# Kernel optimization log

Measured on AMD Instinct MI355X. Metric: run time of the kernel, lower is better.

Reference implementation:

```python
import jax, jax.numpy as jnp
import numpy as np

# ---- dims (match init_kwargs / input_specs) ----
B, T_H, NR = 32, 128, 1      # batch, rollout horizon t, n_ref (= n_x = n_y)
L, D, H = 6, 128, 4          # n_layer, n_embd, n_head
T = T_H + 1                  # GPT sequence buffer length (U has t+1 entries)
DH = D // H
STD = 0.02


def setup_inputs() -> dict:
    key = jax.random.key(0)
    ks = jax.random.split(key, 16)
    p = {}
    p["data"] = jax.random.uniform(ks[0], (B, 2), jnp.float32)          # plant params p0, p1
    p["r"] = jax.random.normal(ks[1], (B, T_H, NR), jnp.float32)        # reference signal
    # GPT params
    p["wte_w"] = jax.random.normal(ks[2], (2 * NR, D), jnp.float32) * STD
    p["wte_b"] = jnp.zeros((D,), jnp.float32)
    p["wpe"] = jax.random.normal(ks[3], (T, D), jnp.float32) * STD
    p["ln1_w"] = jnp.ones((L, D), jnp.float32)
    p["ln1_b"] = jnp.zeros((L, D), jnp.float32)
    p["ln2_w"] = jnp.ones((L, D), jnp.float32)
    p["ln2_b"] = jnp.zeros((L, D), jnp.float32)
    p["qkv_w"] = jax.random.normal(ks[4], (L, D, 3 * D), jnp.float32) * STD
    p["qkv_b"] = jnp.zeros((L, 3 * D), jnp.float32)
    p["attn_proj_w"] = jax.random.normal(ks[5], (L, D, D), jnp.float32) * STD
    p["attn_proj_b"] = jnp.zeros((L, D), jnp.float32)
    p["fc_w"] = jax.random.normal(ks[6], (L, D, 4 * D), jnp.float32) * STD
    p["fc_b"] = jnp.zeros((L, 4 * D), jnp.float32)
    p["fc2_w"] = jax.random.normal(ks[7], (L, 4 * D, D), jnp.float32) * STD
    p["fc2_b"] = jnp.zeros((L, D), jnp.float32)
    p["lnf_w"] = jnp.ones((D,), jnp.float32)
    p["lnf_b"] = jnp.zeros((D,), jnp.float32)
    p["head_w"] = jax.random.normal(ks[8], (D, NR), jnp.float32) * STD
    p["head_b"] = jnp.zeros((NR,), jnp.float32)
    return p


def _ln(x, w, b):
    m = jnp.mean(x, axis=-1, keepdims=True)
    v = jnp.var(x, axis=-1, keepdims=True)
    return (x - m) * jax.lax.rsqrt(v + 1e-5) * w + b


def reference(data, r, wte_w, wte_b, wpe, ln1_w, ln1_b, ln2_w, ln2_b,
              qkv_w, qkv_b, attn_proj_w, attn_proj_b, fc_w, fc_b,
              fc2_w, fc2_b, lnf_w, lnf_b, head_w, head_b):
    causal = jnp.tril(jnp.ones((T, T), bool))
    scale = 1.0 / np.sqrt(DH)

    def gpt(E, U):
        # E, U: [B, T, NR] zero-padded buffers; causal attention makes pos i
        # depend only on filled positions 0..i (identical to prefix forward).
        x = jnp.concatenate([E, U], axis=-1) @ wte_w + wte_b + wpe[None]  # [B,T,D]
        for l in range(L):
            h = _ln(x, ln1_w[l], ln1_b[l])
            qkv = h @ qkv_w[l] + qkv_b[l]
            q, k, v = jnp.split(qkv, 3, axis=-1)
            q = q.reshape(B, T, H, DH)
            k = k.reshape(B, T, H, DH)
            v = v.reshape(B, T, H, DH)
            att = jnp.einsum('bqhd,bkhd->bhqk', q, k) * scale
            att = jnp.where(causal[None, None], att, -1e9)
            att = jax.nn.softmax(att, axis=-1)
            o = jnp.einsum('bhqk,bkhd->bqhd', att, v).reshape(B, T, D)
            x = x + o @ attn_proj_w[l] + attn_proj_b[l]
            h2 = _ln(x, ln2_w[l], ln2_b[l])
            x = x + jax.nn.gelu(h2 @ fc_w[l] + fc_b[l]) @ fc2_w[l] + fc2_b[l]
        x = _ln(x, lnf_w, lnf_b)
        return x @ head_w + head_b  # [B, T, NR]

    p0 = data[:, 0:1]  # [B,1]
    p1 = data[:, 1:2]

    def step(carry, i):
        E, U, Y, s = carry          # s == y_i == x_i (nx == ny)
        e_i = jnp.take(r, i, axis=1) - s       # [B, NR]
        Y = Y.at[:, i].set(s)
        E = E.at[:, i].set(e_i)
        pred = gpt(E, U)
        u_next = jnp.take(pred, i, axis=1)     # last valid position == i
        U = U.at[:, i + 1].set(u_next)
        # ODE plant: Euler step with Ts = 1
        z = p0 * s                               # intermediate_vars
        x_dot = -z + p1 * jnp.tanh(u_next)       # dynamics
        s_next = s + 1.0 * x_dot
        return (E, U, Y, s_next), None

    E0 = jnp.zeros((B, T, NR), jnp.float32)
    U0 = jnp.zeros((B, T, NR), jnp.float32)    # U[:, 0] = 0
    Y0 = jnp.zeros((B, T_H, NR), jnp.float32)
    s0 = jnp.zeros((B, NR), jnp.float32)
    (E, U, Y, s), _ = jax.lax.scan(step, (E0, U0, Y0, s0), jnp.arange(T_H))
    return Y
```

## Files before the change

### kernel.cpp

```cpp
#include <hip/hip_runtime.h>
#include <math.h>

#define NB   32
#define TH   128
#define NL   6
#define DD   128
#define NH   4
#define DHD  32
#define TCAP 128
#define D3   384
#define D4   512

typedef _Float16 f16;
typedef _Float16 f16x4 __attribute__((ext_vector_type(4)));
typedef _Float16 f16x8 __attribute__((ext_vector_type(8)));

__global__ void prep_kernel(const float* __restrict__ qkv, const float* __restrict__ proj,
                            const float* __restrict__ fc,  const float* __restrict__ fc2,
                            f16* __restrict__ out) {
    int i = blockIdx.x * blockDim.x + threadIdx.x;
    const int n0 = NL * DD * D3, n1 = NL * DD * DD, n2 = NL * DD * D4, n3 = NL * D4 * DD;
    const int total = n0 + n1 + n2 + n3;
    if (i >= total) return;
    float v;
    if (i < n0)                 v = qkv[i];
    else if (i < n0 + n1)       v = proj[i - n0];
    else if (i < n0 + n1 + n2)  v = fc[i - n0 - n1];
    else                        v = fc2[i - n0 - n1 - n2];
    out[i] = (f16)v;
}

template<int CTRL>
__device__ __forceinline__ float dpp_add_f(float v) {
    int t = __builtin_amdgcn_update_dpp(0, __float_as_int(v), CTRL, 0xF, 0xF, true);
    return v + __int_as_float(t);
}
template<int CTRL>
__device__ __forceinline__ float dpp_max_f(float v) {
    int iv = __float_as_int(v);
    int t = __builtin_amdgcn_update_dpp(iv, iv, CTRL, 0xF, 0xF, false);
    return fmaxf(v, __int_as_float(t));
}
__device__ __forceinline__ float wave_sum_bcast(float v) {
    v = dpp_add_f<0x111>(v); v = dpp_add_f<0x112>(v);
    v = dpp_add_f<0x114>(v); v = dpp_add_f<0x118>(v);
    v = dpp_add_f<0x142>(v); v = dpp_add_f<0x143>(v);
    return __int_as_float(__builtin_amdgcn_readlane(__float_as_int(v), 63));
}
__device__ __forceinline__ float wave_max_bcast(float v) {
    v = dpp_max_f<0x111>(v); v = dpp_max_f<0x112>(v);
    v = dpp_max_f<0x114>(v); v = dpp_max_f<0x118>(v);
    v = dpp_max_f<0x142>(v); v = dpp_max_f<0x143>(v);
    return __int_as_float(__builtin_amdgcn_readlane(__float_as_int(v), 63));
}
__device__ __forceinline__ float red8_16_32(float v) {
    v = dpp_add_f<0x108>(v);
    v += __shfl_xor(v, 16);
    v += __shfl_xor(v, 32);
    return v;
}
__device__ __forceinline__ float red4_32(float v) {
    v = dpp_add_f<0x104>(v);
    v = dpp_add_f<0x108>(v);
    v += __shfl_xor(v, 16);
    v += __shfl_xor(v, 32);
    return v;
}

__device__ __forceinline__ float gelu_tanh(float v) {
    float t = v * v * v;
    return 0.5f * v * (1.f + tanhf(0.7978845608028654f * (v + 0.044715f * t)));
}

__device__ __forceinline__ void bar_lds() {
    asm volatile("s_waitcnt lgkmcnt(0)" ::: "memory");
    __builtin_amdgcn_s_barrier();
    asm volatile("" ::: "memory");
}
__device__ __forceinline__ void bar_step() {
    asm volatile("s_waitcnt vmcnt(0) lgkmcnt(0)" ::: "memory");
    __builtin_amdgcn_s_barrier();
    asm volatile("" ::: "memory");
}

__global__ __launch_bounds__(512, 1) void gpt_loop(
    const float* __restrict__ data,  const float* __restrict__ r,
    const float* __restrict__ wte_w, const float* __restrict__ wte_b,
    const float* __restrict__ wpe,
    const float* __restrict__ ln1_w, const float* __restrict__ ln1_b,
    const float* __restrict__ ln2_w, const float* __restrict__ ln2_b,
    const float* __restrict__ qkv_b, const float* __restrict__ proj_b,
    const float* __restrict__ fc_b,  const float* __restrict__ fc2_b,
    const float* __restrict__ lnf_w, const float* __restrict__ lnf_b,
    const float* __restrict__ head_w,const float* __restrict__ head_b,
    const f16* __restrict__ Wq, const f16* __restrict__ Wp,
    const f16* __restrict__ Wf, const f16* __restrict__ Wf2,
    f16* __restrict__ Kc, f16* __restrict__ Vc,
    float* __restrict__ Y)
{
    const int b    = blockIdx.x;
    const int tid  = threadIdx.x;
    const int lane = tid & 63;
    const int wid  = tid >> 6;

    __shared__ __align__(16) float xb[2][DD];
    __shared__ __align__(16) float qv[DD], o[DD], hmid[D4];
    __shared__ __align__(16) float sc[NH][TCAP];
    __shared__ __align__(16) f16 kvK[DD], kvV[DD];
    __shared__ __align__(16) float c_ln1w[NL][DD], c_ln1b[NL][DD], c_ln2w[NL][DD], c_ln2b[NL][DD];
    __shared__ __align__(16) float c_qkvb[NL][D3], c_projb[NL][DD], c_fcb[NL][D4], c_fc2b[NL][DD];
    __shared__ __align__(16) float c_lnfw[DD], c_lnfb[DD], c_headw[DD], c_wte0[DD], c_wte1[DD], c_wteb[DD];

    const float p0 = data[b * 2 + 0];
    const float p1 = data[b * 2 + 1];
    const float hb = head_b[0];

    f16* Kb = Kc + (size_t)b * NL * TCAP * DD;
    f16* Vb = Vc + (size_t)b * NL * TCAP * DD;

    for (int idx = tid; idx < NL * DD; idx += 512) {
        int l = idx / DD, d = idx % DD;
        c_ln1w[l][d] = ln1_w[idx]; c_ln1b[l][d] = ln1_b[idx];
        c_ln2w[l][d] = ln2_w[idx]; c_ln2b[l][d] = ln2_b[idx];
        c_projb[l][d] = proj_b[idx]; c_fc2b[l][d] = fc2_b[idx];
    }
    for (int idx = tid; idx < NL * D3; idx += 512) c_qkvb[idx / D3][idx % D3] = qkv_b[idx];
    for (int idx = tid; idx < NL * D4; idx += 512) c_fcb[idx / D4][idx % D4] = fc_b[idx];
    if (tid < DD) {
        c_lnfw[tid] = lnf_w[tid]; c_lnfb[tid] = lnf_b[tid]; c_headw[tid] = head_w[tid];
        c_wte0[tid] = wte_w[tid]; c_wte1[tid] = wte_w[DD + tid]; c_wteb[tid] = wte_b[tid];
    }
    {
        float4 z4 = make_float4(0.f, 0.f, 0.f, 0.f);
        float4* K4 = (float4*)Kb; float4* V4 = (float4*)Vb;
        const int n4 = NL * TCAP * DD * 2 / 16;
        for (int idx = tid; idx < n4; idx += 512) { K4[idx] = z4; V4[idx] = z4; }
    }
    __syncthreads();

    float s_reg = 0.f;
    if (wid == 0) {
        float e0 = r[b * TH + 0];
        xb[0][lane]      = e0 * c_wte0[lane]      + c_wteb[lane]      + wpe[lane];
        xb[0][lane + 64] = e0 * c_wte0[lane + 64] + c_wteb[lane + 64] + wpe[64 + lane];
    }

    const int cgq = lane & 7, ksq = lane >> 3;
    const int cbq = wid * 64 + cgq * 8, k0q = ksq * 16;
    const int hh  = wid - 4;
    const int vcg = lane & 3, vjs = lane >> 2;
    const int pcg = lane & 31, pks = lane >> 5;
    const int fcg = lane & 15, fks = lane >> 4;

    f16x8 wq[16];
    if (wid < 6) {
        const f16* W = Wq + cbq;
        #pragma unroll
        for (int k = 0; k < 16; k++) wq[k] = *(const f16x8*)(W + (size_t)(k0q + k) * D3);
    }
    __syncthreads();

    for (int i = 0; i < TH; i++) {
        const int inext = (i + 1 < TH) ? (i + 1) : (TH - 1);
        float r_next = r[b * TH + inext];
        float wpe_a  = wpe[(i + 1) * DD + lane];
        float wpe_b  = wpe[(i + 1) * DD + 64 + lane];

        for (int l = 0; l < NL; l++) {
            const int pl = l & 1;
            float* xcur = xb[pl];
            float* xnxt = xb[1 - pl];
            f16* Krow = Kb + ((size_t)l * TCAP + i) * DD;
            f16* Vrow = Vb + ((size_t)l * TCAP + i) * DD;
            const f16* Kl = Kb + (size_t)l * TCAP * DD;
            const f16* Vl = Vb + (size_t)l * TCAP * DD;

            if (wid >= 6) {
                xnxt[(wid - 6) * 64 + lane] = 0.f;
            } else {
                float v0 = xcur[lane], v1 = xcur[lane + 64];
                float sm = wave_sum_bcast(v0 + v1);
                float sq = wave_sum_bcast(v0 * v0 + v1 * v1);
                float m  = sm * (1.f / DD);
                float rs = rsqrtf(sq * (1.f / DD) - m * m + 1e-5f);
                float hk[16];
                #pragma unroll
                for (int t = 0; t < 4; t++) {
                    float4 xx = *(const float4*)&xcur[k0q + 4 * t];
                    float4 ww = *(const float4*)&c_ln1w[l][k0q + 4 * t];
                    float4 bb = *(const float4*)&c_ln1b[l][k0q + 4 * t];
                    hk[4 * t + 0] = (xx.x - m) * rs * ww.x + bb.x;
                    hk[4 * t + 1] = (xx.y - m) * rs * ww.y + bb.y;
                    hk[4 * t + 2] = (xx.z - m) * rs * ww.z + bb.z;
                    hk[4 * t + 3] = (xx.w - m) * rs * ww.w + bb.w;
                }
                float acc[8] = {0.f,0.f,0.f,0.f,0.f,0.f,0.f,0.f};
                #pragma unroll
                for (int k = 0; k < 16; k++) {
                    f16x8 w = wq[k];
                    float hkk = hk[k];
                    #pragma unroll
                    for (int j = 0; j < 8; j++) acc[j] += hkk * (float)w[j];
                }
                #pragma unroll
                for (int j = 0; j < 8; j++) acc[j] = red8_16_32(acc[j]);
                if (ksq == 0) {
                    if (cbq < DD) {
                        #pragma unroll
                        for (int j = 0; j < 8; j++) qv[cbq + j] = acc[j] + c_qkvb[l][cbq + j];
                    } else if (cbq < 2 * DD) {
                        f16x8 kv;
                        #pragma unroll
                        for (int j = 0; j < 8; j++) kv[j] = (f16)(acc[j] + c_qkvb[l][cbq + j]);
                        *(f16x8*)(Krow + (cbq - DD)) = kv;
                        *(f16x8*)(&kvK[cbq - DD])   = kv;
                    } else {
                        f16x8 vv;
                        #pragma unroll
                        for (int j = 0; j < 8; j++) vv[j] = (f16)(acc[j] + c_qkvb[l][cbq + j]);
                        *(f16x8*)(Vrow + (cbq - 2 * DD)) = vv;
                        *(f16x8*)(&kvV[cbq - 2 * DD])   = vv;
                    }
                }
            }
            f16x4 wpt[16];
            if (wid >= 4) {
                const f16* W = Wp + (size_t)l * DD * DD + (size_t)(hh * DHD + pks * 16) * DD + pcg * 4;
                #pragma unroll
                for (int k = 0; k < 16; k++) wpt[k] = *(const f16x4*)(W + (size_t)k * DD);
            }
            bar_lds();

            f16x8 wfh1[8], wfh2[8];
            if (wid < 4) {
                const f16* W2 = Wf + (size_t)l * DD * D4 + cbq;
                #pragma unroll
                for (int k = 0; k < 8; k++) wfh1[k] = *(const f16x8*)(W2 + (size_t)(k0q + k) * D4);
                #pragma unroll
                for (int k = 0; k < 8; k++) wfh2[k] = *(const f16x8*)(W2 + (size_t)(k0q + 8 + k) * D4);
            } else {
                const int im1 = (i > 0) ? (i - 1) : 0;
                const int j0 = (lane < i) ? lane : im1;
                const int j1 = (lane + 64 < i) ? (lane + 64) : im1;
                const f16* K0p = Kl + (size_t)j0 * DD + hh * DHD;
                const f16* K1p = Kl + (size_t)j1 * DD + hh * DHD;
                f16x8 kr0[4], kr1[4];
                #pragma unroll
                for (int g = 0; g < 4; g++) {
                    kr0[g] = *(const f16x8*)(K0p + g * 8);
                    kr1[g] = *(const f16x8*)(K1p + g * 8);
                }
                if (lane == i) {
                    #pragma unroll
                    for (int g = 0; g < 4; g++) kr0[g] = *(const f16x8*)(&kvK[hh * DHD + g * 8]);
                }
                if (lane + 64 == i) {
                    #pragma unroll
                    for (int g = 0; g < 4; g++) kr1[g] = *(const f16x8*)(&kvK[hh * DHD + g * 8]);
                }
                float d0 = 0.f, d1 = 0.f;
                #pragma unroll
                for (int g = 0; g < 4; g++) {
                    f16x8 ka = kr0[g], kb2 = kr1[g];
                    float4 qa = *(const float4*)&qv[hh * DHD + g * 8];
                    float4 qb = *(const float4*)&qv[hh * DHD + g * 8 + 4];
                    d0 += qa.x*(float)ka[0] + qa.y*(float)ka[1] + qa.z*(float)ka[2] + qa.w*(float)ka[3]
                        + qb.x*(float)ka[4] + qb.y*(float)ka[5] + qb.z*(float)ka[6] + qb.w*(float)ka[7];
                    d1 += qa.x*(float)kb2[0] + qa.y*(float)kb2[1] + qa.z*(float)kb2[2] + qa.w*(float)kb2[3]
                        + qb.x*(float)kb2[4] + qb.y*(float)kb2[5] + qb.z*(float)kb2[6] + qb.w*(float)kb2[7];
                }
                f16x8 vreg[8];
                const f16* Vp = Vl + hh * DHD + vcg * 8;
                #pragma unroll
                for (int t = 0; t < 8; t++) {
                    int row = vjs * 8 + t; row = (row < i) ? row : im1;
                    vreg[t] = *(const f16x8*)(Vp + (size_t)row * DD);
                }
                #pragma unroll
                for (int t = 0; t < 8; t++) {
                    if (vjs * 8 + t == i) vreg[t] = *(const f16x8*)(&kvV[hh * DHD + vcg * 8]);
                }
                const float sscale = 0.17677669529663687f;
                const bool ok0 = (lane <= i), ok1 = (lane + 64 <= i);
                float s0 = ok0 ? d0 * sscale : -1e30f;
                float s1 = ok1 ? d1 * sscale : -1e30f;
                float mx = wave_max_bcast(fmaxf(s0, s1));
                float e0 = ok0 ? expf(s0 - mx) : 0.f;
                float e1 = ok1 ? expf(s1 - mx) : 0.f;
                float inv = 1.f / wave_sum_bcast(e0 + e1);
                sc[hh][lane]      = e0 * inv;
                sc[hh][lane + 64] = e1 * inv;
                __builtin_amdgcn_wave_barrier();
                const int ja = vjs * 8;
                float4 pa = *(const float4*)&sc[hh][ja];
                float4 pb = *(const float4*)&sc[hh][ja + 4];
                float pv[8] = {pa.x, pa.y, pa.z, pa.w, pb.x, pb.y, pb.z, pb.w};
                float a[8] = {0.f,0.f,0.f,0.f,0.f,0.f,0.f,0.f};
                #pragma unroll
                for (int t = 0; t < 8; t++) {
                    f16x8 vv = vreg[t];
                    float p = pv[t];
                    #pragma unroll
                    for (int u = 0; u < 8; u++) a[u] += p * (float)vv[u];
                }
                #pragma unroll
                for (int u = 0; u < 8; u++) a[u] = red4_32(a[u]);
                if (vjs == 0) {
                    #pragma unroll
                    for (int u = 0; u < 8; u++) o[hh * DHD + vcg * 8 + u] = a[u];
                }
                __builtin_amdgcn_wave_barrier();
                float ov[16];
                #pragma unroll
                for (int t = 0; t < 4; t++) {
                    float4 q4 = *(const float4*)&o[hh * DHD + pks * 16 + 4 * t];
                    ov[4 * t + 0] = q4.x; ov[4 * t + 1] = q4.y;
                    ov[4 * t + 2] = q4.z; ov[4 * t + 3] = q4.w;
                }
                float ap[4] = {0.f,0.f,0.f,0.f};
                #pragma unroll
                for (int k = 0; k < 16; k++) {
                    f16x4 w = wpt[k];
                    float okk = ov[k];
                    #pragma unroll
                    for (int j = 0; j < 4; j++) ap[j] += okk * (float)w[j];
                }
                #pragma unroll
                for (int j = 0; j < 4; j++) ap[j] += __shfl_xor(ap[j], 32);
                if (pks == 0) {
                    #pragma unroll
                    for (int j = 0; j < 4; j++)
                        atomicAdd(&xcur[pcg * 4 + j],
                                  ap[j] + (hh == 0 ? c_projb[l][pcg * 4 + j] : 0.f));
                }
                const f16* W2 = Wf + (size_t)l * DD * D4 + cbq;
                #pragma unroll
                for (int k = 0; k < 8; k++) wfh1[k] = *(const f16x8*)(W2 + (size_t)(k0q + k) * D4);
                #pragma unroll
                for (int k = 0; k < 8; k++) wfh2[k] = *(const f16x8*)(W2 + (size_t)(k0q + 8 + k) * D4);
            }
            bar_lds();

            {
                float v0 = xcur[lane], v1 = xcur[lane + 64];
                float sm = wave_sum_bcast(v0 + v1);
                float sq = wave_sum_bcast(v0 * v0 + v1 * v1);
                float m  = sm * (1.f / DD);
                float rs = rsqrtf(sq * (1.f / DD) - m * m + 1e-5f);
                float hk[16];
                #pragma unroll
                for (int t = 0; t < 4; t++) {
                    float4 xx = *(const float4*)&xcur[k0q + 4 * t];
                    float4 ww = *(const float4*)&c_ln2w[l][k0q + 4 * t];
                    float4 bb = *(const float4*)&c_ln2b[l][k0q + 4 * t];
                    hk[4 * t + 0] = (xx.x - m) * rs * ww.x + bb.x;
                    hk[4 * t + 1] = (xx.y - m) * rs * ww.y + bb.y;
                    hk[4 * t + 2] = (xx.z - m) * rs * ww.z + bb.z;
                    hk[4 * t + 3] = (xx.w - m) * rs * ww.w + bb.w;
                }
                float acc[8] = {0.f,0.f,0.f,0.f,0.f,0.f,0.f,0.f};
                #pragma unroll
                for (int k = 0; k < 8; k++) {
                    f16x8 w = wfh1[k];
                    float hkk = hk[k];
                    #pragma unroll
                    for (int j = 0; j < 8; j++) acc[j] += hkk * (float)w[j];
                }
                #pragma unroll
                for (int k = 0; k < 8; k++) {
                    f16x8 w = wfh2[k];
                    float hkk = hk[8 + k];
                    #pragma unroll
                    for (int j = 0; j < 8; j++) acc[j] += hkk * (float)w[j];
                }
                f16x8 wf2t[16];
                {
                    const f16* W3 = Wf2 + (size_t)l * D4 * DD + (size_t)(wid * 64 + fks * 16) * DD + fcg * 8;
                    #pragma unroll
                    for (int k = 0; k < 16; k++) wf2t[k] = *(const f16x8*)(W3 + (size_t)k * DD);
                }
                #pragma unroll
                for (int j = 0; j < 8; j++) acc[j] = red8_16_32(acc[j]);
                if (ksq == 0) {
                    #pragma unroll
                    for (int j = 0; j < 8; j++) hmid[cbq + j] = gelu_tanh(acc[j] + c_fcb[l][cbq + j]);
                }
                __builtin_amdgcn_wave_barrier();
                float hv[16];
                #pragma unroll
                for (int t = 0; t < 4; t++) {
                    float4 m4 = *(const float4*)&hmid[wid * 64 + fks * 16 + 4 * t];
                    hv[4 * t + 0] = m4.x; hv[4 * t + 1] = m4.y;
                    hv[4 * t + 2] = m4.z; hv[4 * t + 3] = m4.w;
                }
                float a2[8] = {0.f,0.f,0.f,0.f,0.f,0.f,0.f,0.f};
                #pragma unroll
                for (int k = 0; k < 16; k++) {
                    f16x8 w = wf2t[k];
                    float hkk = hv[k];
                    #pragma unroll
                    for (int j = 0; j < 8; j++) a2[j] += hkk * (float)w[j];
                }
                {
                    const int ln = (l + 1 == NL) ? 0 : (l + 1);
                    if (wid < 6) {
                        const f16* W = Wq + (size_t)ln * DD * D3 + cbq;
                        #pragma unroll
                        for (int k = 0; k < 16; k++) wq[k] = *(const f16x8*)(W + (size_t)(k0q + k) * D3);
                    }
                }
                #pragma unroll
                for (int j = 0; j < 8; j++) {
                    a2[j] += __shfl_xor(a2[j], 16);
                    a2[j] += __shfl_xor(a2[j], 32);
                }
                if (fks == 0) {
                    #pragma unroll
                    for (int j = 0; j < 8; j++)
                        atomicAdd(&xnxt[fcg * 8 + j],
                                  a2[j] + (wid == 0 ? xcur[fcg * 8 + j] + c_fc2b[l][fcg * 8 + j] : 0.f));
                }
            }
            bar_lds();
        }

        if (wid == 0) {
            float v0 = xb[0][lane], v1 = xb[0][lane + 64];
            float sm = wave_sum_bcast(v0 + v1);
            float sq = wave_sum_bcast(v0 * v0 + v1 * v1);
            float m  = sm * (1.f / DD);
            float rs = rsqrtf(sq * (1.f / DD) - m * m + 1e-5f);
            float h0 = (v0 - m) * rs * c_lnfw[lane]      + c_lnfb[lane];
            float h1 = (v1 - m) * rs * c_lnfw[lane + 64] + c_lnfb[lane + 64];
            float v  = wave_sum_bcast(h0 * c_headw[lane] + h1 * c_headw[lane + 64]);
            float un = v + hb;
            float s  = s_reg;
            if (lane == 0) Y[b * TH + i] = s;
            float sn = s + (-p0 * s + p1 * tanhf(un));
            s_reg = sn;
            float e = r_next - sn;
            xb[0][lane]      = e * c_wte0[lane]      + un * c_wte1[lane]      + c_wteb[lane]      + wpe_a;
            xb[0][lane + 64] = e * c_wte0[lane + 64] + un * c_wte1[lane + 64] + c_wteb[lane + 64] + wpe_b;
        }
        bar_step();
    }
}

extern "C" void kernel_launch(void* const* d_in, const int* in_sizes, int n_in,
                              void* d_out, int out_size, void* d_ws, size_t ws_size,
                              hipStream_t stream) {
    const float* data   = (const float*)d_in[0];
    const float* r      = (const float*)d_in[1];
    const float* wte_w  = (const float*)d_in[2];
    const float* wte_b  = (const float*)d_in[3];
    const float* wpe    = (const float*)d_in[4];
    const float* ln1_w  = (const float*)d_in[5];
    const float* ln1_b  = (const float*)d_in[6];
    const float* ln2_w  = (const float*)d_in[7];
    const float* ln2_b  = (const float*)d_in[8];
    const float* qkv_w  = (const float*)d_in[9];
    const float* qkv_b  = (const float*)d_in[10];
    const float* proj_w = (const float*)d_in[11];
    const float* proj_b = (const float*)d_in[12];
    const float* fc_w   = (const float*)d_in[13];
    const float* fc_b   = (const float*)d_in[14];
    const float* fc2_w  = (const float*)d_in[15];
    const float* fc2_b  = (const float*)d_in[16];
    const float* lnf_w  = (const float*)d_in[17];
    const float* lnf_b  = (const float*)d_in[18];
    const float* head_w = (const float*)d_in[19];
    const float* head_b = (const float*)d_in[20];

    f16* wsp = (f16*)d_ws;
    f16* Wq  = wsp;
    f16* Wp  = Wq  + NL * DD * D3;
    f16* Wf  = Wp  + NL * DD * DD;
    f16* Wf2 = Wf  + NL * DD * D4;
    f16* Kc  = Wf2 + NL * D4 * DD;
    f16* Vc  = Kc  + (size_t)NB * NL * TCAP * DD;

    const int n_w = NL * DD * D3 + NL * DD * DD + NL * DD * D4 + NL * D4 * DD;
    prep_kernel<<<(n_w + 255) / 256, 256, 0, stream>>>(qkv_w, proj_w, fc_w, fc2_w, Wq);

    gpt_loop<<<NB, 512, 0, stream>>>(
        data, r, wte_w, wte_b, wpe, ln1_w, ln1_b, ln2_w, ln2_b,
        qkv_b, proj_b, fc_b, fc2_b, lnf_w, lnf_b, head_w, head_b,
        Wq, Wp, Wf, Wf2, Kc, Vc, (float*)d_out);
}
```

Baseline: 7.343 ms.

## Double block size to 1024 threads and repartition GEMV work across 16 waves

The per-batch persistent kernel moves from 8 to 16 wavefronts. Each GEMV (QKV, FC, FC2, attention V) is remapped so a lane handles 8 K-rows instead of 16. Cross-lane reductions become pure DPP row reductions instead of DPP plus shuffles. The goal is to halve the serial per-lane work on the latency-bound token loop, at the cost of more barrier participants, higher register pressure under the 1024-thread bound, and more LDS atomics.

```diff
diff --git a/kernel.cpp b/kernel.cpp
--- a/kernel.cpp
+++ b/kernel.cpp
@@ -53,17 +53,13 @@
     v = dpp_max_f<0x142>(v); v = dpp_max_f<0x143>(v);
     return __int_as_float(__builtin_amdgcn_readlane(__float_as_int(v), 63));
 }
-__device__ __forceinline__ float red8_16_32(float v) {
-    v = dpp_add_f<0x108>(v);
-    v += __shfl_xor(v, 16);
-    v += __shfl_xor(v, 32);
+__device__ __forceinline__ float red_k16(float v) {
+    v = dpp_add_f<0x101>(v); v = dpp_add_f<0x102>(v);
+    v = dpp_add_f<0x104>(v); v = dpp_add_f<0x108>(v);
     return v;
 }
-__device__ __forceinline__ float red4_32(float v) {
-    v = dpp_add_f<0x104>(v);
-    v = dpp_add_f<0x108>(v);
-    v += __shfl_xor(v, 16);
-    v += __shfl_xor(v, 32);
+__device__ __forceinline__ float red_k4(float v) {
+    v = dpp_add_f<0x101>(v); v = dpp_add_f<0x102>(v);
     return v;
 }
 
@@ -83,7 +79,7 @@
     asm volatile("" ::: "memory");
 }
 
-__global__ __launch_bounds__(512, 1) void gpt_loop(
+__global__ __launch_bounds__(1024, 1) void gpt_loop(
     const float* __restrict__ data,  const float* __restrict__ r,
     const float* __restrict__ wte_w, const float* __restrict__ wte_b,
     const float* __restrict__ wpe,
@@ -118,14 +114,14 @@
     f16* Kb = Kc + (size_t)b * NL * TCAP * DD;
     f16* Vb = Vc + (size_t)b * NL * TCAP * DD;
 
-    for (int idx = tid; idx < NL * DD; idx += 512) {
+    for (int idx = tid; idx < NL * DD; idx += 1024) {
         int l = idx / DD, d = idx % DD;
         c_ln1w[l][d] = ln1_w[idx]; c_ln1b[l][d] = ln1_b[idx];
         c_ln2w[l][d] = ln2_w[idx]; c_ln2b[l][d] = ln2_b[idx];
         c_projb[l][d] = proj_b[idx]; c_fc2b[l][d] = fc2_b[idx];
     }
-    for (int idx = tid; idx < NL * D3; idx += 512) c_qkvb[idx / D3][idx % D3] = qkv_b[idx];
-    for (int idx = tid; idx < NL * D4; idx += 512) c_fcb[idx / D4][idx % D4] = fc_b[idx];
+    for (int idx = tid; idx < NL * D3; idx += 1024) c_qkvb[idx / D3][idx % D3] = qkv_b[idx];
+    for (int idx = tid; idx < NL * D4; idx += 1024) c_fcb[idx / D4][idx % D4] = fc_b[idx];
     if (tid < DD) {
         c_lnfw[tid] = lnf_w[tid]; c_lnfb[tid] = lnf_b[tid]; c_headw[tid] = head_w[tid];
         c_wte0[tid] = wte_w[tid]; c_wte1[tid] = wte_w[DD + tid]; c_wteb[tid] = wte_b[tid];
@@ -134,7 +130,7 @@
         float4 z4 = make_float4(0.f, 0.f, 0.f, 0.f);
         float4* K4 = (float4*)Kb; float4* V4 = (float4*)Vb;
         const int n4 = NL * TCAP * DD * 2 / 16;
-        for (int idx = tid; idx < n4; idx += 512) { K4[idx] = z4; V4[idx] = z4; }
+        for (int idx = tid; idx < n4; idx += 1024) { K4[idx] = z4; V4[idx] = z4; }
     }
     __syncthreads();
 
@@ -145,18 +141,19 @@
         xb[0][lane + 64] = e0 * c_wte0[lane + 64] + c_wteb[lane + 64] + wpe[64 + lane];
     }
 
-    const int cgq = lane & 7, ksq = lane >> 3;
-    const int cbq = wid * 64 + cgq * 8, k0q = ksq * 16;
+    const int kls = lane & 15;
+    const int chi = lane >> 4;
+    const int cb  = wid * 32 + chi * 8;
+    const int k0  = kls * 8;
     const int hh  = wid - 4;
-    const int vcg = lane & 3, vjs = lane >> 2;
     const int pcg = lane & 31, pks = lane >> 5;
-    const int fcg = lane & 15, fks = lane >> 4;
-
-    f16x8 wq[16];
-    if (wid < 6) {
-        const f16* W = Wq + cbq;
+    const int f2k = lane & 3,  f2c = lane >> 2;
+
+    f16x8 wq[8];
+    if (wid < 12) {
+        const f16* W = Wq + cb;
         #pragma unroll
-        for (int k = 0; k < 16; k++) wq[k] = *(const f16x8*)(W + (size_t)(k0q + k) * D3);
+        for (int k = 0; k < 8; k++) wq[k] = *(const f16x8*)(W + (size_t)(k0 + k) * D3);
     }
     __syncthreads();
 
@@ -175,69 +172,76 @@
             const f16* Kl = Kb + (size_t)l * TCAP * DD;
             const f16* Vl = Vb + (size_t)l * TCAP * DD;
 
-            if (wid >= 6) {
-                xnxt[(wid - 6) * 64 + lane] = 0.f;
-            } else {
-                float v0 = xcur[lane], v1 = xcur[lane + 64];
-                float sm = wave_sum_bcast(v0 + v1);
-                float sq = wave_sum_bcast(v0 * v0 + v1 * v1);
-                float m  = sm * (1.f / DD);
-                float rs = rsqrtf(sq * (1.f / DD) - m * m + 1e-5f);
-                float hk[16];
-                #pragma unroll
-                for (int t = 0; t < 4; t++) {
-                    float4 xx = *(const float4*)&xcur[k0q + 4 * t];
-                    float4 ww = *(const float4*)&c_ln1w[l][k0q + 4 * t];
-                    float4 bb = *(const float4*)&c_ln1b[l][k0q + 4 * t];
-                    hk[4 * t + 0] = (xx.x - m) * rs * ww.x + bb.x;
-                    hk[4 * t + 1] = (xx.y - m) * rs * ww.y + bb.y;
-                    hk[4 * t + 2] = (xx.z - m) * rs * ww.z + bb.z;
-                    hk[4 * t + 3] = (xx.w - m) * rs * ww.w + bb.w;
-                }
+            if (wid < 12) {
+                float4 xa = *(const float4*)&xcur[k0];
+                float4 xb4 = *(const float4*)&xcur[k0 + 4];
+                float xv[8] = {xa.x, xa.y, xa.z, xa.w, xb4.x, xb4.y, xb4.z, xb4.w};
+                float s8 = 0.f, q8 = 0.f;
+                #pragma unroll
+                for (int t = 0; t < 8; t++) { s8 += xv[t]; q8 += xv[t] * xv[t]; }
+                float m  = wave_sum_bcast(s8) * (1.f / 512.f);
+                float sq = wave_sum_bcast(q8) * (1.f / 512.f);
+                float rs = rsqrtf(sq - m * m + 1e-5f);
+                float4 lw1 = *(const float4*)&c_ln1w[l][k0];
+                float4 lw2 = *(const float4*)&c_ln1w[l][k0 + 4];
+                float4 lb1 = *(const float4*)&c_ln1b[l][k0];
+                float4 lb2 = *(const float4*)&c_ln1b[l][k0 + 4];
+                float lw[8] = {lw1.x,lw1.y,lw1.z,lw1.w,lw2.x,lw2.y,lw2.z,lw2.w};
+                float lb[8] = {lb1.x,lb1.y,lb1.z,lb1.w,lb2.x,lb2.y,lb2.z,lb2.w};
+                float hk[8];
+                #pragma unroll
+                for (int t = 0; t < 8; t++) hk[t] = (xv[t] - m) * rs * lw[t] + lb[t];
                 float acc[8] = {0.f,0.f,0.f,0.f,0.f,0.f,0.f,0.f};
                 #pragma unroll
-                for (int k = 0; k < 16; k++) {
+                for (int k = 0; k < 8; k++) {
                     f16x8 w = wq[k];
                     float hkk = hk[k];
                     #pragma unroll
                     for (int j = 0; j < 8; j++) acc[j] += hkk * (float)w[j];
                 }
                 #pragma unroll
-                for (int j = 0; j < 8; j++) acc[j] = red8_16_32(acc[j]);
-                if (ksq == 0) {
-                    if (cbq < DD) {
+                for (int j = 0; j < 8; j++) acc[j] = red_k16(acc[j]);
+                if (kls == 0) {
+                    if (wid < 4) {
                         #pragma unroll
-                        for (int j = 0; j < 8; j++) qv[cbq + j] = acc[j] + c_qkvb[l][cbq + j];
-                    } else if (cbq < 2 * DD) {
+                        for (int j = 0; j < 8; j++) qv[cb + j] = acc[j] + c_qkvb[l][cb + j];
+                    } else if (wid < 8) {
                         f16x8 kv;
                         #pragma unroll
-                        for (int j = 0; j < 8; j++) kv[j] = (f16)(acc[j] + c_qkvb[l][cbq + j]);
-                        *(f16x8*)(Krow + (cbq - DD)) = kv;
-                        *(f16x8*)(&kvK[cbq - DD])   = kv;
+                        for (int j = 0; j < 8; j++) kv[j] = (f16)(acc[j] + c_qkvb[l][cb + j]);
+                        *(f16x8*)(Krow + (cb - DD)) = kv;
+                        *(f16x8*)(&kvK[cb - DD])   = kv;
                     } else {
                         f16x8 vv;
                         #pragma unroll
-                        for (int j = 0; j < 8; j++) vv[j] = (f16)(acc[j] + c_qkvb[l][cbq + j]);
-                        *(f16x8*)(Vrow + (cbq - 2 * DD)) = vv;
-                        *(f16x8*)(&kvV[cbq - 2 * DD])   = vv;
+                        for (int j = 0; j < 8; j++) vv[j] = (f16)(acc[j] + c_qkvb[l][cb + j]);
+                        *(f16x8*)(Vrow + (cb - 2 * DD)) = vv;
+                        *(f16x8*)(&kvV[cb - 2 * DD])   = vv;
                     }
                 }
+            } else {
+                int t = (wid - 12) * 64 + lane;
+                if (t < DD) xnxt[t] = 0.f;
             }
             f16x4 wpt[16];
-            if (wid >= 4) {
+            if (wid >= 4 && wid < 8) {
                 const f16* W = Wp + (size_t)l * DD * DD + (size_t)(hh * DHD + pks * 16) * DD + pcg * 4;
                 #pragma unroll
                 for (int k = 0; k < 16; k++) wpt[k] = *(const f16x4*)(W + (size_t)k * DD);
             }
             bar_lds();
 
-            f16x8 wfh1[8], wfh2[8];
-            if (wid < 4) {
-                const f16* W2 = Wf + (size_t)l * DD * D4 + cbq;
-                #pragma unroll
-                for (int k = 0; k < 8; k++) wfh1[k] = *(const f16x8*)(W2 + (size_t)(k0q + k) * D4);
-                #pragma unroll
-                for (int k = 0; k < 8; k++) wfh2[k] = *(const f16x8*)(W2 + (size_t)(k0q + 8 + k) * D4);
+            f16x8 wfh[8];
+            if (wid < 4 || wid >= 8) {
+                const f16* W2 = Wf + (size_t)l * DD * D4 + cb;
+                #pragma unroll
+                for (int k = 0; k < 8; k++) wfh[k] = *(const f16x8*)(W2 + (size_t)(k0 + k) * D4);
+                if (wid < 12) {
+                    const int ln = (l + 1 == NL) ? 0 : (l + 1);
+                    const f16* W = Wq + (size_t)ln * DD * D3 + cb;
+                    #pragma unroll
+                    for (int k = 0; k < 8; k++) wq[k] = *(const f16x8*)(W + (size_t)(k0 + k) * D3);
+                }
             } else {
                 const int im1 = (i > 0) ? (i - 1) : 0;
                 const int j0 = (lane < i) ? lane : im1;
@@ -270,15 +274,15 @@
                         + qb.x*(float)kb2[4] + qb.y*(float)kb2[5] + qb.z*(float)kb2[6] + qb.w*(float)kb2[7];
                 }
                 f16x8 vreg[8];
-                const f16* Vp = Vl + hh * DHD + vcg * 8;
+                const f16* Vp = Vl + hh * DHD + chi * 8;
                 #pragma unroll
                 for (int t = 0; t < 8; t++) {
-                    int row = vjs * 8 + t; row = (row < i) ? row : im1;
+                    int row = k0 + t; row = (row < i) ? row : im1;
                     vreg[t] = *(const f16x8*)(Vp + (size_t)row * DD);
                 }
                 #pragma unroll
                 for (int t = 0; t < 8; t++) {
-                    if (vjs * 8 + t == i) vreg[t] = *(const f16x8*)(&kvV[hh * DHD + vcg * 8]);
+                    if (k0 + t == i) vreg[t] = *(const f16x8*)(&kvV[hh * DHD + chi * 8]);
                 }
                 const float sscale = 0.17677669529663687f;
                 const bool ok0 = (lane <= i), ok1 = (lane + 64 <= i);
@@ -291,9 +295,8 @@
                 sc[hh][lane]      = e0 * inv;
                 sc[hh][lane + 64] = e1 * inv;
                 __builtin_amdgcn_wave_barrier();
-                const int ja = vjs * 8;
-                float4 pa = *(const float4*)&sc[hh][ja];
-                float4 pb = *(const float4*)&sc[hh][ja + 4];
+                float4 pa = *(const float4*)&sc[hh][k0];
+                float4 pb = *(const float4*)&sc[hh][k0 + 4];
                 float pv[8] = {pa.x, pa.y, pa.z, pa.w, pb.x, pb.y, pb.z, pb.w};
                 float a[8] = {0.f,0.f,0.f,0.f,0.f,0.f,0.f,0.f};
                 #pragma unroll
@@ -304,10 +307,10 @@
                     for (int u = 0; u < 8; u++) a[u] += p * (float)vv[u];
                 }
                 #pragma unroll
-                for (int u = 0; u < 8; u++) a[u] = red4_32(a[u]);
-                if (vjs == 0) {
-                    #pragma unroll
-                    for (int u = 0; u < 8; u++) o[hh * DHD + vcg * 8 + u] = a[u];
+                for (int u = 0; u < 8; u++) a[u] = red_k16(a[u]);
+                if (kls == 0) {
+                    #pragma unroll
+                    for (int u = 0; u < 8; u++) o[hh * DHD + chi * 8 + u] = a[u];
                 }
                 __builtin_amdgcn_wave_barrier();
                 float ov[16];
@@ -333,92 +336,76 @@
                         atomicAdd(&xcur[pcg * 4 + j],
                                   ap[j] + (hh == 0 ? c_projb[l][pcg * 4 + j] : 0.f));
                 }
-                const f16* W2 = Wf + (size_t)l * DD * D4 + cbq;
-                #pragma unroll
-                for (int k = 0; k < 8; k++) wfh1[k] = *(const f16x8*)(W2 + (size_t)(k0q + k) * D4);
-                #pragma unroll
-                for (int k = 0; k < 8; k++) wfh2[k] = *(const f16x8*)(W2 + (size_t)(k0q + 8 + k) * D4);
+                const f16* W2 = Wf + (size_t)l * DD * D4 + cb;
+                #pragma unroll
+                for (int k = 0; k < 8; k++) wfh[k] = *(const f16x8*)(W2 + (size_t)(k0 + k) * D4);
+                {
+                    const int ln = (l + 1 == NL) ? 0 : (l + 1);
+                    const f16* W = Wq + (size_t)ln * DD * D3 + cb;
+                    #pragma unroll
+                    for (int k = 0; k < 8; k++) wq[k] = *(const f16x8*)(W + (size_t)(k0 + k) * D3);
+                }
             }
             bar_lds();
 
             {
-                float v0 = xcur[lane], v1 = xcur[lane + 64];
-                float sm = wave_sum_bcast(v0 + v1);
-                float sq = wave_sum_bcast(v0 * v0 + v1 * v1);
-                float m  = sm * (1.f / DD);
-                float rs = rsqrtf(sq * (1.f / DD) - m * m + 1e-5f);
-                float hk[16];
-                #pragma unroll
-                for (int t = 0; t < 4; t++) {
-                    float4 xx = *(const float4*)&xcur[k0q + 4 * t];
-                    float4 ww = *(const float4*)&c_ln2w[l][k0q + 4 * t];
-                    float4 bb = *(const float4*)&c_ln2b[l][k0q + 4 * t];
-                    hk[4 * t + 0] = (xx.x - m) * rs * ww.x + bb.x;
-                    hk[4 * t + 1] = (xx.y - m) * rs * ww.y + bb.y;
-                    hk[4 * t + 2] = (xx.z - m) * rs * ww.z + bb.z;
-                    hk[4 * t + 3] = (xx.w - m) * rs * ww.w + bb.w;
-                }
+                float4 xa = *(const float4*)&xcur[k0];
+                float4 xb4 = *(const float4*)&xcur[k0 + 4];
+                float xv[8] = {xa.x, xa.y, xa.z, xa.w, xb4.x, xb4.y, xb4.z, xb4.w};
+                float s8 = 0.f, q8 = 0.f;
+                #pragma unroll
+                for (int t = 0; t < 8; t++) { s8 += xv[t]; q8 += xv[t] * xv[t]; }
+                float m  = wave_sum_bcast(s8) * (1.f / 512.f);
+                float sq = wave_sum_bcast(q8) * (1.f / 512.f);
+                float rs = rsqrtf(sq - m * m + 1e-5f);
+                float4 lw1 = *(const float4*)&c_ln2w[l][k0];
+                float4 lw2 = *(const float4*)&c_ln2w[l][k0 + 4];
+                float4 lb1 = *(const float4*)&c_ln2b[l][k0];
+                float4 lb2 = *(const float4*)&c_ln2b[l][k0 + 4];
+                float lw[8] = {lw1.x,lw1.y,lw1.z,lw1.w,lw2.x,lw2.y,lw2.z,lw2.w};
+                float lb[8] = {lb1.x,lb1.y,lb1.z,lb1.w,lb2.x,lb2.y,lb2.z,lb2.w};
+                float hk[8];
+                #pragma unroll
+                for (int t = 0; t < 8; t++) hk[t] = (xv[t] - m) * rs * lw[t] + lb[t];
                 float acc[8] = {0.f,0.f,0.f,0.f,0.f,0.f,0.f,0.f};
                 #pragma unroll
                 for (int k = 0; k < 8; k++) {
-                    f16x8 w = wfh1[k];
+                    f16x8 w = wfh[k];
                     float hkk = hk[k];
                     #pragma unroll
                     for (int j = 0; j < 8; j++) acc[j] += hkk * (float)w[j];
                 }
+                f16x8 wf2t[8];
+                {
+                    const f16* W3 = Wf2 + (size_t)l * D4 * DD + (size_t)(wid * 32 + f2k * 8) * DD + f2c * 8;
+                    #pragma unroll
+                    for (int t = 0; t < 8; t++) wf2t[t] = *(const f16x8*)(W3 + (size_t)t * DD);
+                }
+                #pragma unroll
+                for (int j = 0; j < 8; j++) acc[j] = red_k16(acc[j]);
+                if (kls == 0) {
+                    #pragma unroll
+                    for (int j = 0; j < 8; j++) hmid[cb + j] = gelu_tanh(acc[j] + c_fcb[l][cb + j]);
+                }
+                __builtin_amdgcn_wave_barrier();
+                float4 m1 = *(const float4*)&hmid[wid * 32 + f2k * 8];
+                float4 m2 = *(const float4*)&hmid[wid * 32 + f2k * 8 + 4];
+                float hv[8] = {m1.x, m1.y, m1.z, m1.w, m2.x, m2.y, m2.z, m2.w};
+                float a2[8] = {0.f,0.f,0.f,0.f,0.f,0.f,0.f,0.f};
                 #pragma unroll
                 for (int k = 0; k < 8; k++) {
-                    f16x8 w = wfh2[k];
-                    float hkk = hk[8 + k];
-                    #pragma unroll
-                    for (int j = 0; j < 8; j++) acc[j] += hkk * (float)w[j];
-                }
-                f16x8 wf2t[16];
-                {
-                    const f16* W3 = Wf2 + (size_t)l * D4 * DD + (size_t)(wid * 64 + fks * 16) * DD + fcg * 8;
-                    #pragma unroll
-                    for (int k = 0; k < 16; k++) wf2t[k] = *(const f16x8*)(W3 + (size_t)k * DD);
-                }
-                #pragma unroll
-                for (int j = 0; j < 8; j++) acc[j] = red8_16_32(acc[j]);
-                if (ksq == 0) {
-                    #pragma unroll
-                    for (int j = 0; j < 8; j++) hmid[cbq + j] = gelu_tanh(acc[j] + c_fcb[l][cbq + j]);
-                }
-                __builtin_amdgcn_wave_barrier();
-                float hv[16];
-                #pragma unroll
-                for (int t = 0; t < 4; t++) {
-                    float4 m4 = *(const float4*)&hmid[wid * 64 + fks * 16 + 4 * t];
-                    hv[4 * t + 0] = m4.x; hv[4 * t + 1] = m4.y;
-                    hv[4 * t + 2] = m4.z; hv[4 * t + 3] = m4.w;
-                }
-                float a2[8] = {0.f,0.f,0.f,0.f,0.f,0.f,0.f,0.f};
-                #pragma unroll
-                for (int k = 0; k < 16; k++) {
                     f16x8 w = wf2t[k];
                     float hkk = hv[k];
                     #pragma unroll
                     for (int j = 0; j < 8; j++) a2[j] += hkk * (float)w[j];
                 }
-                {
-                    const int ln = (l + 1 == NL) ? 0 : (l + 1);
-                    if (wid < 6) {
-                        const f16* W = Wq + (size_t)ln * DD * D3 + cbq;
-                        #pragma unroll
-                        for (int k = 0; k < 16; k++) wq[k] = *(const f16x8*)(W + (size_t)(k0q + k) * D3);
-                    }
-                }
-                #pragma unroll
-                for (int j = 0; j < 8; j++) {
-                    a2[j] += __shfl_xor(a2[j], 16);
-                    a2[j] += __shfl_xor(a2[j], 32);
-                }
-                if (fks == 0) {
+                #pragma unroll
+                for (int j = 0; j < 8; j++) a2[j] = red_k4(a2[j]);
+                if (f2k == 0) {
                     #pragma unroll
                     for (int j = 0; j < 8; j++)
-                        atomicAdd(&xnxt[fcg * 8 + j],
-                                  a2[j] + (wid == 0 ? xcur[fcg * 8 + j] + c_fc2b[l][fcg * 8 + j] : 0.f));
+                        atomicAdd(&xnxt[f2c * 8 + j],
+                                  a2[j] + (wid == 0 ? xcur[f2c * 8 + j] + c_fc2b[l][f2c * 8 + j] : 0.f));
                 }
             }
             bar_lds();
@@ -482,7 +469,7 @@
     const int n_w = NL * DD * D3 + NL * DD * DD + NL * DD * D4 + NL * D4 * DD;
     prep_kernel<<<(n_w + 255) / 256, 256, 0, stream>>>(qkv_w, proj_w, fc_w, fc2_w, Wq);
 
-    gpt_loop<<<NB, 512, 0, stream>>>(
+    gpt_loop<<<NB, 1024, 0, stream>>>(
         data, r, wte_w, wte_b, wpe, ln1_w, ln1_b, ln2_w, ln2_b,
         qkv_b, proj_b, fc_b, fc2_b, lnf_w, lnf_b, head_w, head_b,
         Wq, Wp, Wf, Wf2, Kc, Vc, (float*)d_out);
```

Result: slower. 22.25 ms (+203.0%).
